# Performance work log

Hardware: AMD Instinct MI355X
Metric: run time of the kernel (lower is better)

Reference implementation:

```python
import jax, jax.numpy as jnp
import numpy as np

B, N, K = 2, 8192, 16
D_IN, D_OUT = 64, 128
D_HALF = D_OUT // 2          # 64
D_ATT = D_HALF + D_IN        # 128
EPS = 1e-5


def _bn(x, g, b, m, v):
    # inference-mode BatchNorm over the last (channel) axis
    return g * (x - m) * jax.lax.rsqrt(v + EPS) + b


def _knn(xyz, k):
    # brute-force knn_point: squared euclidean distances, k smallest
    sq = jnp.sum(xyz * xyz, axis=-1)                              # [B,N]
    d2 = sq[:, :, None] + sq[:, None, :] - 2.0 * jnp.einsum('bnc,bmc->bnm', xyz, xyz)
    _, idx = jax.lax.top_k(-d2, k)                                # [B,N,K]
    return idx


_gather = jax.vmap(lambda pts, idx: pts[idx])  # ([N,C],[N,K]) -> [N,K,C]


def setup_inputs() -> dict:
    key = jax.random.key(0)
    ks = jax.random.split(key, 24)
    rn = lambda k, s, sc=0.05: jax.random.normal(k, s, jnp.float32) * sc
    bn_params = lambda k, c: (
        1.0 + rn(jax.random.fold_in(k, 0), (c,), 0.1),   # gamma
        rn(jax.random.fold_in(k, 1), (c,), 0.1),          # beta
        rn(jax.random.fold_in(k, 2), (c,), 0.1),          # running mean
        jax.random.uniform(jax.random.fold_in(k, 3), (c,), jnp.float32, 0.5, 1.5),  # running var
    )
    g1, b1, m1, v1 = bn_params(ks[4], D_HALF)
    g2, b2, m2, v2 = bn_params(ks[5], D_HALF)
    ga, ba, ma, va = bn_params(ks[6], D_OUT)
    gs, bs, ms, vs = bn_params(ks[7], D_OUT)
    return {
        'xyz': jax.random.uniform(ks[0], (B, N, 3), jnp.float32),
        'features': rn(ks[1], (B, N, D_IN), 1.0),
        'w_loc1': rn(ks[2], (D_HALF, 10)),
        'g1': g1, 'b1': b1, 'm1': m1, 'v1': v1,
        'w_loc2': rn(ks[3], (D_HALF, D_HALF)),
        'g2': g2, 'b2': b2, 'm2': m2, 'v2': v2,
        'w_score': rn(ks[8], (D_ATT, D_ATT)),
        'w_att': rn(ks[9], (D_OUT, D_ATT)),
        'ga': ga, 'ba': ba, 'ma': ma, 'va': va,
        'w_sc': rn(ks[10], (D_OUT, D_IN)),
        'gs': gs, 'bs': bs, 'ms': ms, 'vs': vs,
    }


def reference(xyz, features, w_loc1, g1, b1, m1, v1, w_loc2, g2, b2, m2, v2,
              w_score, w_att, ga, ba, ma, va, w_sc, gs, bs, ms, vs):
    # shortcut branch: 1x1 conv1d + BN, [B,N,D_OUT]
    shortcut = _bn(jnp.einsum('bnc,oc->bno', features, w_sc), gs, bs, ms, vs)

    # KNN gather (note: original also computes an identical unused knn + locse_feat; dead code skipped)
    knn_idx = _knn(xyz, K)                       # [B,N,K]
    neighbor_xyz = _gather(xyz, knn_idx)         # [B,N,K,3]
    neighbor_feat = _gather(features, knn_idx)   # [B,N,K,D_IN]

    xyz_tile = jnp.broadcast_to(xyz[:, :, None, :], (B, N, K, 3))
    relative_xyz = neighbor_xyz - xyz_tile
    dist = jnp.sum(relative_xyz * relative_xyz, axis=-1, keepdims=True)
    spatial = jnp.concatenate([xyz_tile, neighbor_xyz, relative_xyz, dist], axis=-1)  # [B,N,K,10]

    # LocSE mlp: two 1x1 conv + BN + ReLU
    h = jax.nn.relu(_bn(jnp.einsum('bnkc,oc->bnko', spatial, w_loc1), g1, b1, m1, v1))
    encoded = jax.nn.relu(_bn(jnp.einsum('bnkc,oc->bnko', h, w_loc2), g2, b2, m2, v2))  # [B,N,K,D_HALF]

    concat = jnp.concatenate([encoded, neighbor_feat], axis=-1)  # [B,N,K,D_ATT]

    # Attentive pooling; NOTE: original uses Softmax(dim=-2) on [B,C,N,K] => softmax over N (axis=1 here)
    scores = jax.nn.softmax(jnp.einsum('bnkc,oc->bnko', concat, w_score), axis=1)
    pooled = jnp.sum(concat * scores, axis=2)                     # [B,N,D_ATT]
    att = jax.nn.relu(_bn(jnp.einsum('bnc,oc->bno', pooled, w_att), ga, ba, ma, va))  # [B,N,D_OUT]

    return jax.nn.relu(att + shortcut)
```

## Files before the change

kernel.cpp:

```cpp
#include <hip/hip_runtime.h>
#include <math.h>

constexpr int kB   = 2;
constexpr int kN   = 8192;
constexpr int kK   = 16;
constexpr int kDIN = 64;
constexpr int kDO  = 128;
constexpr float kEPS = 1e-5f;

typedef short bf16x8 __attribute__((ext_vector_type(8)));
typedef float f32x4  __attribute__((ext_vector_type(4)));
typedef unsigned long long u64;
typedef unsigned int u32;

__device__ __forceinline__ unsigned short f2bf(float f) {
  unsigned u = __float_as_uint(f);
  u = (u + 0x7fffu + ((u >> 16) & 1u)) >> 16;
  return (unsigned short)u;
}
__device__ __forceinline__ unsigned packbf2(float a, float b) {
  return (unsigned)f2bf(a) | ((unsigned)f2bf(b) << 16);
}
__device__ __forceinline__ float bf2f(unsigned short u) {
  return __uint_as_float(((unsigned)u) << 16);
}
__device__ __forceinline__ bf16x8 gfrag8(const float* __restrict__ p) {
  float4 v0 = *reinterpret_cast<const float4*>(p);
  float4 v1 = *reinterpret_cast<const float4*>(p + 4);
  bf16x8 r;
  r[0] = (short)f2bf(v0.x); r[1] = (short)f2bf(v0.y);
  r[2] = (short)f2bf(v0.z); r[3] = (short)f2bf(v0.w);
  r[4] = (short)f2bf(v1.x); r[5] = (short)f2bf(v1.y);
  r[6] = (short)f2bf(v1.z); r[7] = (short)f2bf(v1.w);
  return r;
}
__device__ __forceinline__ bf16x8 ldfrag(const uint4* __restrict__ tab, int idx, int t) {
  uint4 v = tab[idx * 256 + t];
  return *reinterpret_cast<bf16x8*>(&v);
}
#define SWZB(row, byte) ((byte) ^ (((row) & 7) << 4))
#define MFMA16 __builtin_amdgcn_mfma_f32_16x16x32_bf16

__global__ __launch_bounds__(256) void k_prep(const float* __restrict__ xyz,
                                              float4* __restrict__ xyzsq,
                                              u32* __restrict__ bins) {
  int i = blockIdx.x * 256 + threadIdx.x;
  if (i >= kB * kN) return;
  float x = xyz[3 * i], y = xyz[3 * i + 1], z = xyz[3 * i + 2];
  float sq = fmaf(x, x, fmaf(y, y, z * z));
  xyzsq[i] = make_float4(x, y, z, sq);
  int bin = (int)(z * 256.0f);
  bin = bin > 255 ? 255 : (bin < 0 ? 0 : bin);
  atomicAdd(&bins[(i >> 13) * 256 + bin], 1u);
}

__global__ __launch_bounds__(256) void k_wprep(const float* __restrict__ w1,
                                               const float* __restrict__ w2,
                                               const float* __restrict__ wscore,
                                               const float* __restrict__ wattn,
                                               const float* __restrict__ wshort,
                                               uint4* __restrict__ wpk1,
                                               uint4* __restrict__ wpk2) {
  int t = threadIdx.x;
  int lane = t & 63, wid = t >> 6;
  int lrow = lane & 15, lkg = lane >> 4;
  int o0 = wid * 16 + lrow, o1 = (wid + 4) * 16 + lrow;
  bf16x8 B1 = {0, 0, 0, 0, 0, 0, 0, 0};
#pragma unroll
  for (int e = 0; e < 8; ++e) {
    int kk = lkg * 8 + e;
    if (kk < 10) B1[e] = (short)f2bf(w1[o0 * 10 + kk]);
  }
  wpk1[0 * 256 + t] = *reinterpret_cast<uint4*>(&B1);
#pragma unroll
  for (int qq = 0; qq < 2; ++qq) {
    bf16x8 f = gfrag8(w2 + (size_t)o0 * 64 + qq * 32 + lkg * 8);
    wpk1[(1 + qq) * 256 + t] = *reinterpret_cast<uint4*>(&f);
  }
#pragma unroll
  for (int qq = 0; qq < 4; ++qq) {
    bf16x8 f0 = gfrag8(wscore + (size_t)o0 * 128 + qq * 32 + lkg * 8);
    bf16x8 f1 = gfrag8(wscore + (size_t)o1 * 128 + qq * 32 + lkg * 8);
    wpk1[(3 + qq) * 256 + t] = *reinterpret_cast<uint4*>(&f0);
    wpk1[(7 + qq) * 256 + t] = *reinterpret_cast<uint4*>(&f1);
    wpk2[(0 + qq) * 256 + t] = *reinterpret_cast<uint4*>(&f0);
    wpk2[(4 + qq) * 256 + t] = *reinterpret_cast<uint4*>(&f1);
    bf16x8 a0 = gfrag8(wattn + (size_t)o0 * 128 + qq * 32 + lkg * 8);
    bf16x8 a1 = gfrag8(wattn + (size_t)o1 * 128 + qq * 32 + lkg * 8);
    wpk2[(8 + qq) * 256 + t] = *reinterpret_cast<uint4*>(&a0);
    wpk2[(12 + qq) * 256 + t] = *reinterpret_cast<uint4*>(&a1);
  }
#pragma unroll
  for (int qq = 0; qq < 2; ++qq) {
    bf16x8 h0 = gfrag8(wshort + (size_t)o0 * 64 + qq * 32 + lkg * 8);
    bf16x8 h1 = gfrag8(wshort + (size_t)o1 * 64 + qq * 32 + lkg * 8);
    wpk2[(16 + qq) * 256 + t] = *reinterpret_cast<uint4*>(&h0);
    wpk2[(18 + qq) * 256 + t] = *reinterpret_cast<uint4*>(&h1);
  }
}

__global__ __launch_bounds__(256) void k_scan(const u32* __restrict__ bins,
                                              u32* __restrict__ binStart,
                                              u32* __restrict__ binRun) {
  __shared__ u32 sb[256];
  int t = threadIdx.x;
  for (int b = 0; b < 2; ++b) {
    u32 cntv = bins[b * 256 + t];
    sb[t] = cntv;
    __syncthreads();
    for (int d = 1; d < 256; d <<= 1) {
      u32 v = (t >= d) ? sb[t - d] : 0u;
      __syncthreads();
      sb[t] += v;
      __syncthreads();
    }
    u32 inc = sb[t];
    binStart[b * 257 + t + 1] = inc;
    if (t == 0) binStart[b * 257] = 0;
    binRun[b * 256 + t] = inc - cntv;
    __syncthreads();
  }
}

__global__ __launch_bounds__(256) void k_scatter(const float4* __restrict__ xyzsq,
                                                 u32* __restrict__ binRun,
                                                 float4* __restrict__ sxyz,
                                                 int* __restrict__ sidx) {
  int i = blockIdx.x * 256 + threadIdx.x;
  if (i >= kB * kN) return;
  float4 p = xyzsq[i];
  int b = i >> 13, n = i & (kN - 1);
  int bin = (int)(p.z * 256.0f);
  bin = bin > 255 ? 255 : (bin < 0 ? 0 : bin);
  u32 pos = atomicAdd(&binRun[b * 256 + bin], 1u);
  sxyz[b * kN + pos] = p;
  sidx[b * kN + pos] = n;
}

__global__ __launch_bounds__(256) void k_knn(const float4* __restrict__ sxyz,
                                             const int* __restrict__ sidx,
                                             const u32* __restrict__ binStart,
                                             int* __restrict__ knn) {
  __shared__ u64 keys[8][256];
  __shared__ u32 cnt[8];
  __shared__ u32 redo;
  int t = threadIdx.x;
  int sq0 = blockIdx.x * 8;
  int b = sq0 >> 13;
  const float4* base = sxyz + b * kN;
  const int* ibase = sidx + b * kN;
  const u32* bs = binStart + b * 257;
  float4 qv[8]; int qo[8];
#pragma unroll
  for (int qq = 0; qq < 8; ++qq) {
    qv[qq] = base[(sq0 & (kN - 1)) + qq];
    qo[qq] = ibase[(sq0 & (kN - 1)) + qq];
  }
  float zmin = qv[0].z, zmax = qv[0].z;
#pragma unroll
  for (int qq = 1; qq < 8; ++qq) {
    zmin = fminf(zmin, qv[qq].z);
    zmax = fmaxf(zmax, qv[qq].z);
  }
  if (t < 8) cnt[t] = 0;
  if (t == 0) redo = 0;
  __syncthreads();
  {
    int blo = (int)floorf((zmin - 0.1265f) * 256.0f); blo = blo < 0 ? 0 : blo;
    int bhi = (int)floorf((zmax + 0.1265f) * 256.0f); bhi = bhi > 255 ? 255 : bhi;
    int jlo = (int)bs[blo], jhi = (int)bs[bhi + 1];
    for (int j = jlo + t; j < jhi; j += 256) {
      float4 c = base[j];
      int jorig = ibase[j];
#pragma unroll
      for (int qq = 0; qq < 8; ++qq) {
        float dot = fmaf(qv[qq].x, c.x, fmaf(qv[qq].y, c.y, qv[qq].z * c.z));
        float d2 = (qv[qq].w + c.w) - 2.0f * dot;
        if (d2 < 0.015625f) {
          u32 u = __float_as_uint(d2);
          u = (u & 0x80000000u) ? ~u : (u | 0x80000000u);
          u32 pos = atomicAdd(&cnt[qq], 1u);
          if (pos < 256u) keys[qq][pos] = ((u64)u << 32) | (u32)jorig;
        }
      }
    }
  }
  __syncthreads();
  if (t < 8 && cnt[t] < 16u) { atomicOr(&redo, 1u << t); cnt[t] = 0; }
  __syncthreads();
  u32 rmask = redo;
  if (rmask) {
    int blo = (int)floorf((zmin - 0.2515f) * 256.0f); blo = blo < 0 ? 0 : blo;
    int bhi = (int)floorf((zmax + 0.2515f) * 256.0f); bhi = bhi > 255 ? 255 : bhi;
    int jlo = (int)bs[blo], jhi = (int)bs[bhi + 1];
    for (int j = jlo + t; j < jhi; j += 256) {
      float4 c = base[j];
      int jorig = ibase[j];
#pragma unroll
      for (int qq = 0; qq < 8; ++qq) {
        if (rmask & (1u << qq)) {
          float dot = fmaf(qv[qq].x, c.x, fmaf(qv[qq].y, c.y, qv[qq].z * c.z));
          float d2 = (qv[qq].w + c.w) - 2.0f * dot;
          if (d2 < 0.0625f) {
            u32 u = __float_as_uint(d2);
            u = (u & 0x80000000u) ? ~u : (u | 0x80000000u);
            u32 pos = atomicAdd(&cnt[qq], 1u);
            if (pos < 256u) keys[qq][pos] = ((u64)u << 32) | (u32)jorig;
          }
        }
      }
    }
    __syncthreads();
  }
  {
    int qq = t >> 5, s0 = t & 31;
    u32 nk = cnt[qq]; if (nk > 256u) nk = 256u;
    for (int s = s0; s < (int)nk; s += 32) {
      u64 myk = keys[qq][s];
      u32 rank = 0;
      for (u32 i2 = 0; i2 < nk; ++i2) rank += (keys[qq][i2] < myk) ? 1u : 0u;
      if (rank < 16u)
        knn[(size_t)(b * kN + qo[qq]) * kK + rank] = (int)(u32)(myk & 0xffffffffu);
    }
  }
}

template <int PASS, bool STASH>
__global__ __launch_bounds__(256) void k_main(
    const float4* __restrict__ xyzsq, const float* __restrict__ feat,
    const int* __restrict__ knn,
    const float* __restrict__ g1, const float* __restrict__ b1,
    const float* __restrict__ m1, const float* __restrict__ v1,
    const float* __restrict__ g2, const float* __restrict__ b2,
    const float* __restrict__ m2, const float* __restrict__ v2,
    const float* __restrict__ ga, const float* __restrict__ ba,
    const float* __restrict__ ma, const float* __restrict__ va,
    const float* __restrict__ gs, const float* __restrict__ bsv,
    const float* __restrict__ ms, const float* __restrict__ vs,
    const uint4* __restrict__ wpk1, const uint4* __restrict__ wpk2,
    float* __restrict__ partials, const float* __restrict__ MZ,
    uint4* __restrict__ ccws,
    float* __restrict__ out, int ppb) {
  constexpr bool kLoadPath = !(PASS == 2 && STASH);
  __shared__ float s1[64], bb1v[64], s2[64], bb2v[64];
  __shared__ float sA[128], bAv[128], sS[128], bSv[128];
  __shared__ alignas(16) char hb[kLoadPath ? 4 * 16 * 128 : 16];
  __shared__ alignas(16) char ccb[4 * 16 * 256];
  __shared__ alignas(16) char pl[PASS == 2 ? 16 * 256 : 16];
  __shared__ alignas(16) float2 mzs[PASS == 2 ? 2048 : 1];

  int t = threadIdx.x;
  int lane = t & 63, wid = t >> 6;
  int lrow = lane & 15, lkg = lane >> 4;
  int p0 = blockIdx.x * ppb;
  int bb = p0 >> 13;
  const int o0 = wid * 16 + lrow, o1 = (wid + 4) * 16 + lrow;

  if (t < 64) {
    float sc1 = g1[t] * rsqrtf(v1[t] + kEPS);
    s1[t] = sc1; bb1v[t] = fmaf(-m1[t], sc1, b1[t]);
    float sc2 = g2[t] * rsqrtf(v2[t] + kEPS);
    s2[t] = sc2; bb2v[t] = fmaf(-m2[t], sc2, b2[t]);
  } else if (t < 192) {
    int o = t - 64;
    float scA = ga[o] * rsqrtf(va[o] + kEPS);
    sA[o] = scA; bAv[o] = fmaf(-ma[o], scA, ba[o]);
    float scS = gs[o] * rsqrtf(vs[o] + kEPS);
    sS[o] = scS; bSv[o] = fmaf(-ms[o], scS, bsv[o]);
  }
  if constexpr (PASS == 2) {
    const float4* src = reinterpret_cast<const float4*>(MZ + (size_t)bb * 4096);
    float4* dst = reinterpret_cast<float4*>(mzs);
    for (int e = t; e < 1024; e += 256) dst[e] = src[e];
  }
  __syncthreads();

  float s1v = 0.f, b1v = 0.f, scv = 0.f, bcv = 0.f;
  if constexpr (kLoadPath) {
    s1v = s1[o0]; b1v = bb1v[o0];
    scv = s2[o0]; bcv = bb2v[o0];
  }

  bf16x8 B1 = {0, 0, 0, 0, 0, 0, 0, 0};
  bf16x8 Bc[2], Bs0[4], Bs1[4], Ba0[4], Ba1[4], Bh0[2], Bh1[2];
  if constexpr (kLoadPath) {
    B1 = ldfrag(wpk1, 0, t);
#pragma unroll
    for (int qq = 0; qq < 2; ++qq) Bc[qq] = ldfrag(wpk1, 1 + qq, t);
#pragma unroll
    for (int qq = 0; qq < 4; ++qq) {
      Bs0[qq] = ldfrag(wpk1, 3 + qq, t);
      Bs1[qq] = ldfrag(wpk1, 7 + qq, t);
    }
  } else {
#pragma unroll
    for (int qq = 0; qq < 4; ++qq) {
      Bs0[qq] = ldfrag(wpk2, 0 + qq, t);
      Bs1[qq] = ldfrag(wpk2, 4 + qq, t);
    }
  }
  if constexpr (PASS == 2) {
#pragma unroll
    for (int qq = 0; qq < 4; ++qq) {
      Ba0[qq] = ldfrag(wpk2, 8 + qq, t);
      Ba1[qq] = ldfrag(wpk2, 12 + qq, t);
    }
#pragma unroll
    for (int qq = 0; qq < 2; ++qq) {
      Bh0[qq] = ldfrag(wpk2, 16 + qq, t);
      Bh1[qq] = ldfrag(wpk2, 18 + qq, t);
    }
  }

  float rm0[4], rz0[4], rm1[4], rz1[4];
#pragma unroll
  for (int r = 0; r < 4; ++r) {
    rm0[r] = -INFINITY; rz0[r] = 0.f;
    rm1[r] = -INFINITY; rz1[r] = 0.f;
  }

  const int ngrp = ppb >> 2;

  for (int gi = 0; gi < ngrp; ++gi) {
    int pg0 = p0 + gi * 4;
    __syncthreads();

    if constexpr (kLoadPath) {
      {
        int ak = t >> 4, ac4 = t & 15;
#pragma unroll
        for (int pp = 0; pp < 4; ++pp) {
          int aj = knn[(pg0 + pp) * kK + ak];
          float4 v = reinterpret_cast<const float4*>(feat + (size_t)(bb * kN + aj) * kDIN)[ac4];
          *reinterpret_cast<uint2*>(ccb + pp * 4096 + SWZB(ak, ak * 256 + 128 + ac4 * 8)) =
              make_uint2(packbf2(v.x, v.y), packbf2(v.z, v.w));
        }
      }
      {
#pragma unroll
        for (int pp = 0; pp < 4; ++pp) {
          int pg = pg0 + pp;
          int n = pg & (kN - 1);
          float4 qc = xyzsq[bb * kN + n];
          bf16x8 A = {0, 0, 0, 0, 0, 0, 0, 0};
          if (lkg < 2) {
            int j = knn[pg * kK + lrow];
            float4 cj = xyzsq[bb * kN + j];
            float rx = cj.x - qc.x, ry = cj.y - qc.y, rzv = cj.z - qc.z;
            if (lkg == 0) {
              A[0] = (short)f2bf(qc.x); A[1] = (short)f2bf(qc.y);
              A[2] = (short)f2bf(qc.z); A[3] = (short)f2bf(cj.x);
              A[4] = (short)f2bf(cj.y); A[5] = (short)f2bf(cj.z);
              A[6] = (short)f2bf(rx);   A[7] = (short)f2bf(ry);
            } else {
              float dist = fmaf(rx, rx, fmaf(ry, ry, rzv * rzv));
              A[0] = (short)f2bf(rzv);  A[1] = (short)f2bf(dist);
            }
          }
          f32x4 zz = {0.f, 0.f, 0.f, 0.f};
          f32x4 hacc = MFMA16(A, B1, zz, 0, 0, 0);
#pragma unroll
          for (int r = 0; r < 4; ++r) {
            int k = lkg * 4 + r;
            float h = fmaxf(fmaf(hacc[r], s1v, b1v), 0.f);
            *reinterpret_cast<unsigned short*>(hb + pp * 2048 + SWZB(k, k * 128 + o0 * 2)) = f2bf(h);
          }
        }
      }
      __syncthreads();
      {
#pragma unroll
        for (int pp = 0; pp < 4; ++pp) {
          f32x4 accc = {0.f, 0.f, 0.f, 0.f};
#pragma unroll
          for (int qq = 0; qq < 2; ++qq) {
            bf16x8 a = *reinterpret_cast<const bf16x8*>(
                hb + pp * 2048 + SWZB(lrow, lrow * 128 + qq * 64 + lkg * 16));
            accc = MFMA16(a, Bc[qq], accc, 0, 0, 0);
          }
#pragma unroll
          for (int r = 0; r < 4; ++r) {
            int k = lkg * 4 + r;
            float e = fmaxf(fmaf(accc[r], scv, bcv), 0.f);
            *reinterpret_cast<unsigned short*>(ccb + pp * 4096 + SWZB(k, k * 256 + o0 * 2)) = f2bf(e);
          }
        }
      }
      __syncthreads();
    } else {
      uint4 cc4[4];
#pragma unroll
      for (int pp = 0; pp < 4; ++pp) cc4[pp] = ccws[(size_t)(pg0 + pp) * 256 + t];
#pragma unroll
      for (int pp = 0; pp < 4; ++pp)
        *reinterpret_cast<uint4*>(ccb + pp * 4096 + t * 16) = cc4[pp];
      __syncthreads();
    }
    {
#pragma unroll
      for (int pp = 0; pp < 4; ++pp) {
        if constexpr (PASS == 1 && STASH) {
          ccws[(size_t)(pg0 + pp) * 256 + t] =
              *reinterpret_cast<const uint4*>(ccb + pp * 4096 + t * 16);
        }
        f32x4 acc0 = {0.f, 0.f, 0.f, 0.f}, acc1 = {0.f, 0.f, 0.f, 0.f};
#pragma unroll
        for (int qq = 0; qq < 4; ++qq) {
          bf16x8 a = *reinterpret_cast<const bf16x8*>(
              ccb + pp * 4096 + SWZB(lrow, lrow * 256 + qq * 64 + lkg * 16));
          acc0 = MFMA16(a, Bs0[qq], acc0, 0, 0, 0);
          acc1 = MFMA16(a, Bs1[qq], acc1, 0, 0, 0);
        }
        if constexpr (PASS == 1) {
#pragma unroll
          for (int r = 0; r < 4; ++r) {
            float sv0 = acc0[r];
            bool up0 = sv0 > rm0[r];
            float e0 = __expf(up0 ? rm0[r] - sv0 : sv0 - rm0[r]);
            rz0[r] = up0 ? fmaf(rz0[r], e0, 1.f) : rz0[r] + e0;
            rm0[r] = up0 ? sv0 : rm0[r];
            float sv1 = acc1[r];
            bool up1 = sv1 > rm1[r];
            float e1 = __expf(up1 ? rm1[r] - sv1 : sv1 - rm1[r]);
            rz1[r] = up1 ? fmaf(rz1[r], e1, 1.f) : rz1[r] + e1;
            rm1[r] = up1 ? sv1 : rm1[r];
          }
        } else {
          float ps0 = 0.f, ps1 = 0.f;
#pragma unroll
          for (int r = 0; r < 4; ++r) {
            int k = lkg * 4 + r;
            float2 mz0 = mzs[k * 128 + o0];
            float2 mz1 = mzs[k * 128 + o1];
            float sc0 = __expf(acc0[r] - mz0.x) * mz0.y;
            float sc1 = __expf(acc1[r] - mz1.x) * mz1.y;
            float c0 = bf2f(*reinterpret_cast<const unsigned short*>(
                ccb + pp * 4096 + SWZB(k, k * 256 + o0 * 2)));
            float c1 = bf2f(*reinterpret_cast<const unsigned short*>(
                ccb + pp * 4096 + SWZB(k, k * 256 + o1 * 2)));
            ps0 = fmaf(c0, sc0, ps0);
            ps1 = fmaf(c1, sc1, ps1);
          }
          ps0 += __shfl_xor(ps0, 16, 64); ps0 += __shfl_xor(ps0, 32, 64);
          ps1 += __shfl_xor(ps1, 16, 64); ps1 += __shfl_xor(ps1, 32, 64);
          int rowpt = (gi * 4 + pp) & 15;
          if (lane < 16) {
            *reinterpret_cast<unsigned short*>(pl + SWZB(rowpt, rowpt * 256 + o0 * 2)) = f2bf(ps0);
            *reinterpret_cast<unsigned short*>(pl + SWZB(rowpt, rowpt * 256 + o1 * 2)) = f2bf(ps1);
          }
        }
      }
    }
    if constexpr (PASS == 2) {
      if ((gi & 3) == 3) {
        __syncthreads();
        int pgE = pg0 + 3;
        f32x4 aa0 = {0.f, 0.f, 0.f, 0.f}, aa1 = {0.f, 0.f, 0.f, 0.f};
        f32x4 as0 = {0.f, 0.f, 0.f, 0.f}, as1 = {0.f, 0.f, 0.f, 0.f};
#pragma unroll
        for (int qq = 0; qq < 4; ++qq) {
          bf16x8 a = *reinterpret_cast<const bf16x8*>(
              pl + SWZB(lrow, lrow * 256 + qq * 64 + lkg * 16));
          aa0 = MFMA16(a, Ba0[qq], aa0, 0, 0, 0);
          aa1 = MFMA16(a, Ba1[qq], aa1, 0, 0, 0);
        }
        int nb0 = (pgE - 15) & (kN - 1);
#pragma unroll
        for (int qq = 0; qq < 2; ++qq) {
          bf16x8 a = gfrag8(feat + (size_t)(bb * kN + nb0 + lrow) * 64 + qq * 32 + lkg * 8);
          as0 = MFMA16(a, Bh0[qq], as0, 0, 0, 0);
          as1 = MFMA16(a, Bh1[qq], as1, 0, 0, 0);
        }
        size_t pbase = (size_t)(pgE - 15) * kDO;
#pragma unroll
        for (int r = 0; r < 4; ++r) {
          int row = lkg * 4 + r;
          float att0 = fmaxf(fmaf(aa0[r], sA[o0], bAv[o0]), 0.f);
          float att1 = fmaxf(fmaf(aa1[r], sA[o1], bAv[o1]), 0.f);
          float sh0 = fmaf(as0[r], sS[o0], bSv[o0]);
          float sh1 = fmaf(as1[r], sS[o1], bSv[o1]);
          out[pbase + (size_t)row * kDO + o0] = fmaxf(att0 + sh0, 0.f);
          out[pbase + (size_t)row * kDO + o1] = fmaxf(att1 + sh1, 0.f);
        }
      }
    }
  }
  if constexpr (PASS == 1) {
    float* pb = partials + (size_t)blockIdx.x * 4096;
#pragma unroll
    for (int r = 0; r < 4; ++r) {
      int k = lkg * 4 + r;
      pb[(k * 128 + o0) * 2]     = rm0[r];
      pb[(k * 128 + o0) * 2 + 1] = rz0[r];
      pb[(k * 128 + o1) * 2]     = rm1[r];
      pb[(k * 128 + o1) * 2 + 1] = rz1[r];
    }
  }
}

__global__ __launch_bounds__(256) void k_merge(const float* __restrict__ partials,
                                               float* __restrict__ MZ, int nb) {
  int wv = (blockIdx.x << 2) | (threadIdx.x >> 6);
  int lane = threadIdx.x & 63;
  if (wv >= kB * kK * kDO) return;
  int b = wv >> 11, rest = wv & 2047;
  int half = nb >> 1;
  const float2* pp = reinterpret_cast<const float2*>(partials);
  float m = -1e30f, z = 0.f;
  for (int i = lane; i < half; i += 64) {
    float2 mz = pp[(size_t)(b * half + i) * 2048 + rest];
    float nm = fmaxf(m, mz.x);
    z = z * __expf(m - nm) + mz.y * __expf(mz.x - nm);
    m = nm;
  }
#pragma unroll
  for (int d = 1; d < 64; d <<= 1) {
    float om = __shfl_xor(m, d, 64);
    float oz = __shfl_xor(z, d, 64);
    float nm = fmaxf(m, om);
    z = z * __expf(m - nm) + oz * __expf(om - nm);
    m = nm;
  }
  if (lane == 0) {
    MZ[(b * 2048 + rest) * 2]     = m;
    MZ[(b * 2048 + rest) * 2 + 1] = 1.0f / z;
  }
}

extern "C" void kernel_launch(void* const* d_in, const int* in_sizes, int n_in,
                              void* d_out, int out_size, void* d_ws, size_t ws_size,
                              hipStream_t stream) {
  (void)in_sizes; (void)n_in; (void)out_size;
  const float* xyz    = (const float*)d_in[0];
  const float* feat   = (const float*)d_in[1];
  const float* w1     = (const float*)d_in[2];
  const float* g1     = (const float*)d_in[3];
  const float* b1     = (const float*)d_in[4];
  const float* m1     = (const float*)d_in[5];
  const float* v1     = (const float*)d_in[6];
  const float* w2     = (const float*)d_in[7];
  const float* g2     = (const float*)d_in[8];
  const float* b2     = (const float*)d_in[9];
  const float* m2     = (const float*)d_in[10];
  const float* v2     = (const float*)d_in[11];
  const float* wscore = (const float*)d_in[12];
  const float* wattn  = (const float*)d_in[13];
  const float* ga     = (const float*)d_in[14];
  const float* ba     = (const float*)d_in[15];
  const float* ma     = (const float*)d_in[16];
  const float* va     = (const float*)d_in[17];
  const float* wshort = (const float*)d_in[18];
  const float* gs     = (const float*)d_in[19];
  const float* bsv    = (const float*)d_in[20];
  const float* ms     = (const float*)d_in[21];
  const float* vs     = (const float*)d_in[22];
  float* out = (float*)d_out;

  char* wsb = (char*)d_ws;
  float4* xyzsq    = (float4*)wsb;
  int*    knn      = (int*)(wsb + 262144);
  float*  MZ       = (float*)(wsb + 1310720);
  float4* sxyz     = (float4*)(wsb + 1343488);
  int*    sidx     = (int*)(wsb + 1605632);
  u32*    bins     = (u32*)(wsb + 1671168);
  u32*    binStart = (u32*)(wsb + 1673216);
  u32*    binRun   = (u32*)(wsb + 1675776);
  uint4*  wpk1     = (uint4*)(wsb + 1677824);
  uint4*  wpk2     = (uint4*)(wsb + 1722880);
  float*  partials = (float*)(wsb + 1804800);
  uint4*  ccws     = (uint4*)(wsb + 18582016);
  constexpr size_t kStashEnd = 18582016ull + 67108864ull;
  bool stash = ws_size >= kStashEnd;
  size_t avail = ws_size > 1804800 ? ws_size - 1804800 : 0;
  int nb = 1024;
  while (nb > 2 && (size_t)nb * 16384ull > avail) nb >>= 1;
  int ppb1 = (kB * kN) / nb;

  hipMemsetAsync(bins, 0, 2048, stream);
  k_prep   <<<64, 256, 0, stream>>>(xyz, xyzsq, bins);
  k_wprep  <<<1, 256, 0, stream>>>(w1, w2, wscore, wattn, wshort, wpk1, wpk2);
  k_scan   <<<1, 256, 0, stream>>>(bins, binStart, binRun);
  k_scatter<<<64, 256, 0, stream>>>(xyzsq, binRun, sxyz, sidx);
  k_knn    <<<kB * kN / 8, 256, 0, stream>>>(sxyz, sidx, binStart, knn);
  if (stash) {
    k_main<1, true><<<nb, 256, 0, stream>>>(xyzsq, feat, knn,
                                            g1, b1, m1, v1, g2, b2, m2, v2,
                                            ga, ba, ma, va, gs, bsv, ms, vs,
                                            wpk1, wpk2,
                                            partials, nullptr, ccws, nullptr, ppb1);
    k_merge<<<1024, 256, 0, stream>>>(partials, MZ, nb);
    k_main<2, true><<<1024, 256, 0, stream>>>(xyzsq, feat, knn,
                                              g1, b1, m1, v1, g2, b2, m2, v2,
                                              ga, ba, ma, va, gs, bsv, ms, vs,
                                              wpk1, wpk2,
                                              nullptr, MZ, ccws, out, 16);
  } else {
    k_main<1, false><<<nb, 256, 0, stream>>>(xyzsq, feat, knn,
                                             g1, b1, m1, v1, g2, b2, m2, v2,
                                             ga, ba, ma, va, gs, bsv, ms, vs,
                                             wpk1, wpk2,
                                             partials, nullptr, ccws, nullptr, ppb1);
    k_merge<<<1024, 256, 0, stream>>>(partials, MZ, nb);
    k_main<2, false><<<1024, 256, 0, stream>>>(xyzsq, feat, knn,
                                               g1, b1, m1, v1, g2, b2, m2, v2,
                                               ga, ba, ma, va, gs, bsv, ms, vs,
                                               wpk1, wpk2,
                                               nullptr, MZ, ccws, out, 16);
  }
}
```

Baseline: 161.0 us.

## Stash exp-weighted concat products and pool with a lightweight second kernel

```diff
diff --git a/kernel.cpp b/kernel.cpp
--- a/kernel.cpp
+++ b/kernel.cpp
@@ -239,12 +239,11 @@
     const float* __restrict__ ms, const float* __restrict__ vs,
     const uint4* __restrict__ wpk1, const uint4* __restrict__ wpk2,
     float* __restrict__ partials, const float* __restrict__ MZ,
-    uint4* __restrict__ ccws,
+    unsigned short* __restrict__ Xws,
     float* __restrict__ out, int ppb) {
-  constexpr bool kLoadPath = !(PASS == 2 && STASH);
   __shared__ float s1[64], bb1v[64], s2[64], bb2v[64];
   __shared__ float sA[128], bAv[128], sS[128], bSv[128];
-  __shared__ alignas(16) char hb[kLoadPath ? 4 * 16 * 128 : 16];
+  __shared__ alignas(16) char hb[4 * 16 * 128];
   __shared__ alignas(16) char ccb[4 * 16 * 256];
   __shared__ alignas(16) char pl[PASS == 2 ? 16 * 256 : 16];
   __shared__ alignas(16) float2 mzs[PASS == 2 ? 2048 : 1];
@@ -275,29 +274,17 @@
   }
   __syncthreads();
 
-  float s1v = 0.f, b1v = 0.f, scv = 0.f, bcv = 0.f;
-  if constexpr (kLoadPath) {
-    s1v = s1[o0]; b1v = bb1v[o0];
-    scv = s2[o0]; bcv = bb2v[o0];
-  }
-
-  bf16x8 B1 = {0, 0, 0, 0, 0, 0, 0, 0};
-  bf16x8 Bc[2], Bs0[4], Bs1[4], Ba0[4], Ba1[4], Bh0[2], Bh1[2];
-  if constexpr (kLoadPath) {
-    B1 = ldfrag(wpk1, 0, t);
-#pragma unroll
-    for (int qq = 0; qq < 2; ++qq) Bc[qq] = ldfrag(wpk1, 1 + qq, t);
-#pragma unroll
-    for (int qq = 0; qq < 4; ++qq) {
-      Bs0[qq] = ldfrag(wpk1, 3 + qq, t);
-      Bs1[qq] = ldfrag(wpk1, 7 + qq, t);
-    }
-  } else {
-#pragma unroll
-    for (int qq = 0; qq < 4; ++qq) {
-      Bs0[qq] = ldfrag(wpk2, 0 + qq, t);
-      Bs1[qq] = ldfrag(wpk2, 4 + qq, t);
-    }
+  float s1v = s1[o0], b1v = bb1v[o0];
+  float scv = s2[o0], bcv = bb2v[o0];
+
+  bf16x8 B1, Bc[2], Bs0[4], Bs1[4], Ba0[4], Ba1[4], Bh0[2], Bh1[2];
+  B1 = ldfrag(wpk1, 0, t);
+#pragma unroll
+  for (int qq = 0; qq < 2; ++qq) Bc[qq] = ldfrag(wpk1, 1 + qq, t);
+#pragma unroll
+  for (int qq = 0; qq < 4; ++qq) {
+    Bs0[qq] = ldfrag(wpk1, 3 + qq, t);
+    Bs1[qq] = ldfrag(wpk1, 7 + qq, t);
   }
   if constexpr (PASS == 2) {
 #pragma unroll
@@ -312,12 +299,9 @@
     }
   }
 
-  float rm0[4], rz0[4], rm1[4], rz1[4];
-#pragma unroll
-  for (int r = 0; r < 4; ++r) {
-    rm0[r] = -INFINITY; rz0[r] = 0.f;
-    rm1[r] = -INFINITY; rz1[r] = 0.f;
-  }
+  float rz0[4], rz1[4];
+#pragma unroll
+  for (int r = 0; r < 4; ++r) { rz0[r] = 0.f; rz1[r] = 0.f; }
 
   const int ngrp = ppb >> 2;
 
@@ -325,84 +309,70 @@
     int pg0 = p0 + gi * 4;
     __syncthreads();
 
-    if constexpr (kLoadPath) {
-      {
-        int ak = t >> 4, ac4 = t & 15;
-#pragma unroll
-        for (int pp = 0; pp < 4; ++pp) {
-          int aj = knn[(pg0 + pp) * kK + ak];
-          float4 v = reinterpret_cast<const float4*>(feat + (size_t)(bb * kN + aj) * kDIN)[ac4];
-          *reinterpret_cast<uint2*>(ccb + pp * 4096 + SWZB(ak, ak * 256 + 128 + ac4 * 8)) =
-              make_uint2(packbf2(v.x, v.y), packbf2(v.z, v.w));
-        }
+    {
+      int ak = t >> 4, ac4 = t & 15;
+#pragma unroll
+      for (int pp = 0; pp < 4; ++pp) {
+        int aj = knn[(pg0 + pp) * kK + ak];
+        float4 v = reinterpret_cast<const float4*>(feat + (size_t)(bb * kN + aj) * kDIN)[ac4];
+        *reinterpret_cast<uint2*>(ccb + pp * 4096 + SWZB(ak, ak * 256 + 128 + ac4 * 8)) =
+            make_uint2(packbf2(v.x, v.y), packbf2(v.z, v.w));
       }
-      {
-#pragma unroll
-        for (int pp = 0; pp < 4; ++pp) {
-          int pg = pg0 + pp;
-          int n = pg & (kN - 1);
-          float4 qc = xyzsq[bb * kN + n];
-          bf16x8 A = {0, 0, 0, 0, 0, 0, 0, 0};
-          if (lkg < 2) {
-            int j = knn[pg * kK + lrow];
-            float4 cj = xyzsq[bb * kN + j];
-            float rx = cj.x - qc.x, ry = cj.y - qc.y, rzv = cj.z - qc.z;
-            if (lkg == 0) {
-              A[0] = (short)f2bf(qc.x); A[1] = (short)f2bf(qc.y);
-              A[2] = (short)f2bf(qc.z); A[3] = (short)f2bf(cj.x);
-              A[4] = (short)f2bf(cj.y); A[5] = (short)f2bf(cj.z);
-              A[6] = (short)f2bf(rx);   A[7] = (short)f2bf(ry);
-            } else {
-              float dist = fmaf(rx, rx, fmaf(ry, ry, rzv * rzv));
-              A[0] = (short)f2bf(rzv);  A[1] = (short)f2bf(dist);
-            }
+    }
+    {
+#pragma unroll
+      for (int pp = 0; pp < 4; ++pp) {
+        int pg = pg0 + pp;
+        int n = pg & (kN - 1);
+        float4 qc = xyzsq[bb * kN + n];
+        bf16x8 A = {0, 0, 0, 0, 0, 0, 0, 0};
+        if (lkg < 2) {
+          int j = knn[pg * kK + lrow];
+          float4 cj = xyzsq[bb * kN + j];
+          float rx = cj.x - qc.x, ry = cj.y - qc.y, rzv = cj.z - qc.z;
+          if (lkg == 0) {
+            A[0] = (short)f2bf(qc.x); A[1] = (short)f2bf(qc.y);
+            A[2] = (short)f2bf(qc.z); A[3] = (short)f2bf(cj.x);
+            A[4] = (short)f2bf(cj.y); A[5] = (short)f2bf(cj.z);
+            A[6] = (short)f2bf(rx);   A[7] = (short)f2bf(ry);
+          } else {
+            float dist = fmaf(rx, rx, fmaf(ry, ry, rzv * rzv));
+            A[0] = (short)f2bf(rzv);  A[1] = (short)f2bf(dist);
           }
-          f32x4 zz = {0.f, 0.f, 0.f, 0.f};
-          f32x4 hacc = MFMA16(A, B1, zz, 0, 0, 0);
-#pragma unroll
-          for (int r = 0; r < 4; ++r) {
-            int k = lkg * 4 + r;
-            float h = fmaxf(fmaf(hacc[r], s1v, b1v), 0.f);
-            *reinterpret_cast<unsigned short*>(hb + pp * 2048 + SWZB(k, k * 128 + o0 * 2)) = f2bf(h);
-          }
+        }
+        f32x4 zz = {0.f, 0.f, 0.f, 0.f};
+        f32x4 hacc = MFMA16(A, B1, zz, 0, 0, 0);
+#pragma unroll
+        for (int r = 0; r < 4; ++r) {
+          int k = lkg * 4 + r;
+          float h = fmaxf(fmaf(hacc[r], s1v, b1v), 0.f);
+          *reinterpret_cast<unsigned short*>(hb + pp * 2048 + SWZB(k, k * 128 + o0 * 2)) = f2bf(h);
         }
       }
-      __syncthreads();
-      {
-#pragma unroll
-        for (int pp = 0; pp < 4; ++pp) {
-          f32x4 accc = {0.f, 0.f, 0.f, 0.f};
-#pragma unroll
-          for (int qq = 0; qq < 2; ++qq) {
-            bf16x8 a = *reinterpret_cast<const bf16x8*>(
-                hb + pp * 2048 + SWZB(lrow, lrow * 128 + qq * 64 + lkg * 16));
-            accc = MFMA16(a, Bc[qq], accc, 0, 0, 0);
-          }
-#pragma unroll
-          for (int r = 0; r < 4; ++r) {
-            int k = lkg * 4 + r;
-            float e = fmaxf(fmaf(accc[r], scv, bcv), 0.f);
-            *reinterpret_cast<unsigned short*>(ccb + pp * 4096 + SWZB(k, k * 256 + o0 * 2)) = f2bf(e);
-          }
+    }
+    __syncthreads();
+    {
+#pragma unroll
+      for (int pp = 0; pp < 4; ++pp) {
+        f32x4 accc = {0.f, 0.f, 0.f, 0.f};
+#pragma unroll
+        for (int qq = 0; qq < 2; ++qq) {
+          bf16x8 a = *reinterpret_cast<const bf16x8*>(
+              hb + pp * 2048 + SWZB(lrow, lrow * 128 + qq * 64 + lkg * 16));
+          accc = MFMA16(a, Bc[qq], accc, 0, 0, 0);
+        }
+#pragma unroll
+        for (int r = 0; r < 4; ++r) {
+          int k = lkg * 4 + r;
+          float e = fmaxf(fmaf(accc[r], scv, bcv), 0.f);
+          *reinterpret_cast<unsigned short*>(ccb + pp * 4096 + SWZB(k, k * 256 + o0 * 2)) = f2bf(e);
         }
       }
-      __syncthreads();
-    } else {
-      uint4 cc4[4];
-#pragma unroll
-      for (int pp = 0; pp < 4; ++pp) cc4[pp] = ccws[(size_t)(pg0 + pp) * 256 + t];
-#pragma unroll
-      for (int pp = 0; pp < 4; ++pp)
-        *reinterpret_cast<uint4*>(ccb + pp * 4096 + t * 16) = cc4[pp];
-      __syncthreads();
-    }
+    }
+    __syncthreads();
     {
 #pragma unroll
       for (int pp = 0; pp < 4; ++pp) {
-        if constexpr (PASS == 1 && STASH) {
-          ccws[(size_t)(pg0 + pp) * 256 + t] =
-              *reinterpret_cast<const uint4*>(ccb + pp * 4096 + t * 16);
-        }
         f32x4 acc0 = {0.f, 0.f, 0.f, 0.f}, acc1 = {0.f, 0.f, 0.f, 0.f};
 #pragma unroll
         for (int qq = 0; qq < 4; ++qq) {
@@ -412,18 +382,29 @@
           acc1 = MFMA16(a, Bs1[qq], acc1, 0, 0, 0);
         }
         if constexpr (PASS == 1) {
+          unsigned short xv0[4], xv1[4];
 #pragma unroll
           for (int r = 0; r < 4; ++r) {
-            float sv0 = acc0[r];
-            bool up0 = sv0 > rm0[r];
-            float e0 = __expf(up0 ? rm0[r] - sv0 : sv0 - rm0[r]);
-            rz0[r] = up0 ? fmaf(rz0[r], e0, 1.f) : rz0[r] + e0;
-            rm0[r] = up0 ? sv0 : rm0[r];
-            float sv1 = acc1[r];
-            bool up1 = sv1 > rm1[r];
-            float e1 = __expf(up1 ? rm1[r] - sv1 : sv1 - rm1[r]);
-            rz1[r] = up1 ? fmaf(rz1[r], e1, 1.f) : rz1[r] + e1;
-            rm1[r] = up1 ? sv1 : rm1[r];
+            int k = lkg * 4 + r;
+            float e0 = __expf(acc0[r]);
+            rz0[r] += e0;
+            float c0 = bf2f(*reinterpret_cast<const unsigned short*>(
+                ccb + pp * 4096 + SWZB(k, k * 256 + o0 * 2)));
+            xv0[r] = f2bf(c0 * e0);
+            float e1 = __expf(acc1[r]);
+            rz1[r] += e1;
+            float c1 = bf2f(*reinterpret_cast<const unsigned short*>(
+                ccb + pp * 4096 + SWZB(k, k * 256 + o1 * 2)));
+            xv1[r] = f2bf(c1 * e1);
+          }
+          if constexpr (STASH) {
+            size_t pg = (size_t)(pg0 + pp);
+            uint2 wa = make_uint2((u32)xv0[0] | ((u32)xv0[1] << 16),
+                                  (u32)xv0[2] | ((u32)xv0[3] << 16));
+            uint2 wb = make_uint2((u32)xv1[0] | ((u32)xv1[1] << 16),
+                                  (u32)xv1[2] | ((u32)xv1[3] << 16));
+            *reinterpret_cast<uint2*>(Xws + ((pg * 128 + o0) * 16 + lkg * 4)) = wa;
+            *reinterpret_cast<uint2*>(Xws + ((pg * 128 + o1) * 16 + lkg * 4)) = wb;
           }
         } else {
           float ps0 = 0.f, ps1 = 0.f;
@@ -486,14 +467,12 @@
     }
   }
   if constexpr (PASS == 1) {
-    float* pb = partials + (size_t)blockIdx.x * 4096;
+    float* pb = partials + (size_t)blockIdx.x * 2048;
 #pragma unroll
     for (int r = 0; r < 4; ++r) {
       int k = lkg * 4 + r;
-      pb[(k * 128 + o0) * 2]     = rm0[r];
-      pb[(k * 128 + o0) * 2 + 1] = rz0[r];
-      pb[(k * 128 + o1) * 2]     = rm1[r];
-      pb[(k * 128 + o1) * 2 + 1] = rz1[r];
+      pb[k * 128 + o0] = rz0[r];
+      pb[k * 128 + o1] = rz1[r];
     }
   }
 }
@@ -505,25 +484,110 @@
   if (wv >= kB * kK * kDO) return;
   int b = wv >> 11, rest = wv & 2047;
   int half = nb >> 1;
-  const float2* pp = reinterpret_cast<const float2*>(partials);
-  float m = -1e30f, z = 0.f;
-  for (int i = lane; i < half; i += 64) {
-    float2 mz = pp[(size_t)(b * half + i) * 2048 + rest];
-    float nm = fmaxf(m, mz.x);
-    z = z * __expf(m - nm) + mz.y * __expf(mz.x - nm);
-    m = nm;
-  }
-#pragma unroll
-  for (int d = 1; d < 64; d <<= 1) {
-    float om = __shfl_xor(m, d, 64);
-    float oz = __shfl_xor(z, d, 64);
-    float nm = fmaxf(m, om);
-    z = z * __expf(m - nm) + oz * __expf(om - nm);
-    m = nm;
-  }
+  float z = 0.f;
+  for (int i = lane; i < half; i += 64)
+    z += partials[(size_t)(b * half + i) * 2048 + rest];
+#pragma unroll
+  for (int d = 1; d < 64; d <<= 1) z += __shfl_xor(z, d, 64);
   if (lane == 0) {
-    MZ[(b * 2048 + rest) * 2]     = m;
+    MZ[(b * 2048 + rest) * 2]     = 0.f;
     MZ[(b * 2048 + rest) * 2 + 1] = 1.0f / z;
+  }
+}
+
+__global__ __launch_bounds__(256) void k_pool(
+    const unsigned short* __restrict__ Xws, const float* __restrict__ MZ,
+    const float* __restrict__ feat, const uint4* __restrict__ wpk2,
+    const float* __restrict__ ga, const float* __restrict__ ba,
+    const float* __restrict__ ma, const float* __restrict__ va,
+    const float* __restrict__ gs, const float* __restrict__ bsv,
+    const float* __restrict__ ms, const float* __restrict__ vs,
+    float* __restrict__ out) {
+  __shared__ float invzL[2048];
+  __shared__ float sA[128], bAv[128], sS[128], bSv[128];
+  __shared__ alignas(16) char pl[16 * 256];
+  int t = threadIdx.x;
+  int lane = t & 63, wid = t >> 6;
+  int lrow = lane & 15, lkg = lane >> 4;
+  int p0 = blockIdx.x * 16;
+  int bb = p0 >> 13;
+  const int o0 = wid * 16 + lrow, o1 = (wid + 4) * 16 + lrow;
+
+  if (t >= 64 && t < 192) {
+    int o = t - 64;
+    float scA = ga[o] * rsqrtf(va[o] + kEPS);
+    sA[o] = scA; bAv[o] = fmaf(-ma[o], scA, ba[o]);
+    float scS = gs[o] * rsqrtf(vs[o] + kEPS);
+    sS[o] = scS; bSv[o] = fmaf(-ms[o], scS, bsv[o]);
+  }
+  {
+    const float2* mzp = reinterpret_cast<const float2*>(MZ) + (size_t)bb * 2048;
+    for (int e = t; e < 2048; e += 256) invzL[e] = mzp[e].y;
+  }
+  bf16x8 Ba0[4], Ba1[4], Bh0[2], Bh1[2];
+#pragma unroll
+  for (int qq = 0; qq < 4; ++qq) {
+    Ba0[qq] = ldfrag(wpk2, 8 + qq, t);
+    Ba1[qq] = ldfrag(wpk2, 12 + qq, t);
+  }
+#pragma unroll
+  for (int qq = 0; qq < 2; ++qq) {
+    Bh0[qq] = ldfrag(wpk2, 16 + qq, t);
+    Bh1[qq] = ldfrag(wpk2, 18 + qq, t);
+  }
+  __syncthreads();
+
+  const int o = t & 127, ph = t >> 7;
+  for (int s8 = 0; s8 < 8; ++s8) {
+    int rowpt = s8 * 2 + ph;
+    size_t pg = (size_t)(p0 + rowpt);
+    const unsigned short* xp = Xws + (pg * 128 + o) * 16;
+    uint4 xa = *reinterpret_cast<const uint4*>(xp);
+    uint4 xb = *reinterpret_cast<const uint4*>(xp + 8);
+    const float* iz = invzL + o;
+    float acc = 0.f;
+#pragma unroll
+    for (int w = 0; w < 4; ++w) {
+      u32 word = (&xa.x)[w];
+      acc = fmaf(bf2f((unsigned short)(word & 0xffffu)), iz[(2 * w) * 128], acc);
+      acc = fmaf(bf2f((unsigned short)(word >> 16)),     iz[(2 * w + 1) * 128], acc);
+    }
+#pragma unroll
+    for (int w = 0; w < 4; ++w) {
+      u32 word = (&xb.x)[w];
+      acc = fmaf(bf2f((unsigned short)(word & 0xffffu)), iz[(8 + 2 * w) * 128], acc);
+      acc = fmaf(bf2f((unsigned short)(word >> 16)),     iz[(9 + 2 * w) * 128], acc);
+    }
+    *reinterpret_cast<unsigned short*>(pl + SWZB(rowpt, rowpt * 256 + o * 2)) = f2bf(acc);
+  }
+  __syncthreads();
+
+  f32x4 aa0 = {0.f, 0.f, 0.f, 0.f}, aa1 = {0.f, 0.f, 0.f, 0.f};
+  f32x4 as0 = {0.f, 0.f, 0.f, 0.f}, as1 = {0.f, 0.f, 0.f, 0.f};
+#pragma unroll
+  for (int qq = 0; qq < 4; ++qq) {
+    bf16x8 a = *reinterpret_cast<const bf16x8*>(
+        pl + SWZB(lrow, lrow * 256 + qq * 64 + lkg * 16));
+    aa0 = MFMA16(a, Ba0[qq], aa0, 0, 0, 0);
+    aa1 = MFMA16(a, Ba1[qq], aa1, 0, 0, 0);
+  }
+  int nb0 = p0 & (kN - 1);
+#pragma unroll
+  for (int qq = 0; qq < 2; ++qq) {
+    bf16x8 a = gfrag8(feat + (size_t)(bb * kN + nb0 + lrow) * 64 + qq * 32 + lkg * 8);
+    as0 = MFMA16(a, Bh0[qq], as0, 0, 0, 0);
+    as1 = MFMA16(a, Bh1[qq], as1, 0, 0, 0);
+  }
+  size_t pbase = (size_t)p0 * kDO;
+#pragma unroll
+  for (int r = 0; r < 4; ++r) {
+    int row = lkg * 4 + r;
+    float att0 = fmaxf(fmaf(aa0[r], sA[o0], bAv[o0]), 0.f);
+    float att1 = fmaxf(fmaf(aa1[r], sA[o1], bAv[o1]), 0.f);
+    float sh0 = fmaf(as0[r], sS[o0], bSv[o0]);
+    float sh1 = fmaf(as1[r], sS[o1], bSv[o1]);
+    out[pbase + (size_t)row * kDO + o0] = fmaxf(att0 + sh0, 0.f);
+    out[pbase + (size_t)row * kDO + o1] = fmaxf(att1 + sh1, 0.f);
   }
 }
 
@@ -568,12 +632,18 @@
   uint4*  wpk1     = (uint4*)(wsb + 1677824);
   uint4*  wpk2     = (uint4*)(wsb + 1722880);
   float*  partials = (float*)(wsb + 1804800);
-  uint4*  ccws     = (uint4*)(wsb + 18582016);
-  constexpr size_t kStashEnd = 18582016ull + 67108864ull;
-  bool stash = ws_size >= kStashEnd;
-  size_t avail = ws_size > 1804800 ? ws_size - 1804800 : 0;
-  int nb = 1024;
-  while (nb > 2 && (size_t)nb * 16384ull > avail) nb >>= 1;
+
+  const size_t kBase = 1804800ull;
+  const size_t kXsz  = 67108864ull;
+  int nb; bool stash;
+  if (ws_size >= kBase + 1024ull * 8192ull + kXsz) { nb = 1024; stash = true; }
+  else {
+    stash = false;
+    size_t avail = ws_size > kBase ? ws_size - kBase : 0;
+    nb = 1024;
+    while (nb > 2 && (size_t)nb * 8192ull > avail) nb >>= 1;
+  }
+  unsigned short* Xws = (unsigned short*)(wsb + kBase + (size_t)nb * 8192ull);
   int ppb1 = (kB * kN) / nb;
 
   hipMemsetAsync(bins, 0, 2048, stream);
@@ -587,24 +657,21 @@
                                             g1, b1, m1, v1, g2, b2, m2, v2,
                                             ga, ba, ma, va, gs, bsv, ms, vs,
                                             wpk1, wpk2,
-                                            partials, nullptr, ccws, nullptr, ppb1);
+                                            partials, nullptr, Xws, nullptr, ppb1);
     k_merge<<<1024, 256, 0, stream>>>(partials, MZ, nb);
-    k_main<2, true><<<1024, 256, 0, stream>>>(xyzsq, feat, knn,
-                                              g1, b1, m1, v1, g2, b2, m2, v2,
-                                              ga, ba, ma, va, gs, bsv, ms, vs,
-                                              wpk1, wpk2,
-                                              nullptr, MZ, ccws, out, 16);
+    k_pool <<<1024, 256, 0, stream>>>(Xws, MZ, feat, wpk2,
+                                      ga, ba, ma, va, gs, bsv, ms, vs, out);
   } else {
     k_main<1, false><<<nb, 256, 0, stream>>>(xyzsq, feat, knn,
                                              g1, b1, m1, v1, g2, b2, m2, v2,
                                              ga, ba, ma, va, gs, bsv, ms, vs,
                                              wpk1, wpk2,
-                                             partials, nullptr, ccws, nullptr, ppb1);
+                                             partials, nullptr, Xws, nullptr, ppb1);
     k_merge<<<1024, 256, 0, stream>>>(partials, MZ, nb);
     k_main<2, false><<<1024, 256, 0, stream>>>(xyzsq, feat, knn,
                                                g1, b1, m1, v1, g2, b2, m2, v2,
                                                ga, ba, ma, va, gs, bsv, ms, vs,
                                                wpk1, wpk2,
-                                               nullptr, MZ, ccws, out, 16);
-  }
-}
+                                               nullptr, MZ, Xws, out, 16);
+  }
+}
```

Measured after the change: 141.3 us. 12.3% less time.
